# Kernel optimization log

Measured on AMD Instinct MI355X. Metric: run time of the kernel, lower is better.

## Reference

```python
import jax, jax.numpy as jnp
import numpy as np
from jax import lax

B, S, D, H_HEADS, K, G, E, HID = 2, 1024, 1024, 16, 31, 4, 2, 2048
HD = D // H_HEADS

def _layer_norm(x, g, b, eps=1e-5):
    mu = jnp.mean(x, axis=-1, keepdims=True)
    var = jnp.mean(jnp.square(x - mu), axis=-1, keepdims=True)
    return (x - mu) * lax.rsqrt(var + eps) * g + b

def setup_inputs() -> dict:
    key = jax.random.key(0)
    ks = jax.random.split(key, 16)
    s = 0.02
    return {
        "x": jax.random.normal(ks[0], (B, S, D), jnp.float32),
        "group_ids": jax.random.randint(ks[1], (B, S), 0, G, jnp.int32),
        "cn_g": jnp.ones((D,), jnp.float32), "cn_b": jnp.zeros((D,), jnp.float32),
        "conv_w": jax.random.normal(ks[2], (D, D, K), jnp.float32) * s,
        "conv_b": jnp.zeros((D,), jnp.float32),
        "an_g": jnp.ones((D,), jnp.float32), "an_b": jnp.zeros((D,), jnp.float32),
        "in_w": jax.random.normal(ks[3], (3 * D, D), jnp.float32) * s,
        "in_b": jnp.zeros((3 * D,), jnp.float32),
        "out_w": jax.random.normal(ks[4], (D, D), jnp.float32) * s,
        "out_b": jnp.zeros((D,), jnp.float32),
        "e_w1": jax.random.normal(ks[5], (G, E, D, HID), jnp.float32) * s,
        "e_b1": jnp.zeros((G, E, HID), jnp.float32),
        "e_w2": jax.random.normal(ks[6], (G, E, HID, D), jnp.float32) * s,
        "e_b2": jnp.zeros((G, E, D), jnp.float32),
    }

def reference(x, group_ids, cn_g, cn_b, conv_w, conv_b, an_g, an_b,
              in_w, in_b, out_w, out_b, e_w1, e_b1, e_w2, e_b2):
    # ---- conv block (dropout off: deterministic/eval) ----
    residual = x
    h = _layer_norm(x, cn_g, cn_b)
    hc = jnp.transpose(h, (0, 2, 1))  # [B, D, S]
    hc = lax.conv_general_dilated(hc, conv_w, window_strides=(1,),
                                  padding=[(K // 2, K // 2)],
                                  dimension_numbers=("NCH", "OIH", "NCH"))
    hc = hc + conv_b[None, :, None]
    hc = jnp.transpose(hc, (0, 2, 1))
    x = jax.nn.gelu(hc, approximate=False) + residual
    # ---- self-attention block ----
    residual = x
    h = _layer_norm(x, an_g, an_b)
    qkv = h @ in_w.T + in_b  # [B, S, 3D]
    q, k, v = jnp.split(qkv, 3, axis=-1)
    q = q.reshape(B, S, H_HEADS, HD)
    k = k.reshape(B, S, H_HEADS, HD)
    v = v.reshape(B, S, H_HEADS, HD)
    scores = jnp.einsum("bqhd,bkhd->bhqk", q, k) / jnp.sqrt(jnp.float32(HD))
    attn = jax.nn.softmax(scores, axis=-1)
    ctx = jnp.einsum("bhqk,bkhd->bqhd", attn, v).reshape(B, S, D)
    x = ctx @ out_w.T + out_b + residual
    # ---- group-routed MoE (dense compute over groups, select by group id) ----
    residual = x
    xf = x.reshape(B * S, D)
    gid = group_ids.reshape(B * S)
    h1 = jax.nn.gelu(jnp.einsum("nd,gedh->ngeh", xf, e_w1) + e_b1, approximate=False)
    out_all = jnp.einsum("ngeh,gehd->nged", h1, e_w2) + e_b2  # [N, G, E, D]
    out_all = jnp.mean(out_all, axis=2)  # mean over experts in group -> [N, G, D]
    sel = jnp.take_along_axis(out_all, gid[:, None, None].astype(jnp.int32), axis=1)[:, 0]
    x = sel.reshape(B, S, D) + residual
    return x
```

## Files before the change

kernel.cpp:

```cpp
#include <hip/hip_runtime.h>
#include <hip/hip_bf16.h>
#include <math.h>

#define BB 2
#define SS 1024
#define DD 1024
#define HH 16
#define HDIM 64
#define KK 31
#define GG 4
#define EE 2
#define HIDN 2048
#define NTOK (BB*SS)
#define D3 (3*DD)

typedef unsigned short u16;
typedef __attribute__((ext_vector_type(8))) short s16x8;
typedef __attribute__((ext_vector_type(8))) unsigned short u16x8;
typedef __attribute__((ext_vector_type(4))) unsigned short u16x4;
typedef __attribute__((ext_vector_type(4))) float f32x4;
typedef __attribute__((ext_vector_type(2))) unsigned int u32x2;

__device__ __forceinline__ float gelu_f(float x) {
  return 0.5f * x * (1.0f + erff(x * 0.7071067811865475f));
}
__device__ __forceinline__ u16 f2bf(float f) {
  unsigned u = __builtin_bit_cast(unsigned, f);
  u = (u + 0x7fffu + ((u >> 16) & 1u)) >> 16;
  return (u16)u;
}
__device__ __forceinline__ float bf2f(u16 u) {
  return __builtin_bit_cast(float, ((unsigned)u) << 16);
}
__device__ __forceinline__ f32x4 MFMA16(s16x8 a, s16x8 b, f32x4 c) {
  return __builtin_amdgcn_mfma_f32_16x16x32_bf16(a, b, c, 0, 0, 0);
}
#define GLOAD16(gp, lp) __builtin_amdgcn_global_load_lds( \
    (const __attribute__((address_space(1))) void*)(gp),  \
    (__attribute__((address_space(3))) void*)(lp), 16, 0, 0)

__global__ void ln_kernel(const float* __restrict__ x, const float* __restrict__ g,
                          const float* __restrict__ b, u16* __restrict__ out) {
  const int row = blockIdx.x;
  const int tid = threadIdx.x;
  __shared__ float red[4];
  const float4 v = reinterpret_cast<const float4*>(x + (size_t)row * DD)[tid];
  float s = v.x + v.y + v.z + v.w;
  s += __shfl_down(s, 32); s += __shfl_down(s, 16); s += __shfl_down(s, 8);
  s += __shfl_down(s, 4);  s += __shfl_down(s, 2);  s += __shfl_down(s, 1);
  if ((tid & 63) == 0) red[tid >> 6] = s;
  __syncthreads();
  const float mean = (red[0] + red[1] + red[2] + red[3]) * (1.0f / DD);
  __syncthreads();
  const float4 d = make_float4(v.x - mean, v.y - mean, v.z - mean, v.w - mean);
  float sq = d.x*d.x + d.y*d.y + d.z*d.z + d.w*d.w;
  sq += __shfl_down(sq, 32); sq += __shfl_down(sq, 16); sq += __shfl_down(sq, 8);
  sq += __shfl_down(sq, 4);  sq += __shfl_down(sq, 2);  sq += __shfl_down(sq, 1);
  if ((tid & 63) == 0) red[tid >> 6] = sq;
  __syncthreads();
  const float var = (red[0] + red[1] + red[2] + red[3]) * (1.0f / DD);
  const float rstd = rsqrtf(var + 1e-5f);
  const float4 gv = reinterpret_cast<const float4*>(g)[tid];
  const float4 bv = reinterpret_cast<const float4*>(b)[tid];
  u16x4 o;
  o[0] = f2bf(d.x * rstd * gv.x + bv.x);
  o[1] = f2bf(d.y * rstd * gv.y + bv.y);
  o[2] = f2bf(d.z * rstd * gv.z + bv.z);
  o[3] = f2bf(d.w * rstd * gv.w + bv.w);
  *reinterpret_cast<u16x4*>(out + (size_t)row * DD + tid * 4) = o;
}

__global__ void prep_convw(const float* __restrict__ cw, u16* __restrict__ Wb) {
  const int o = blockIdx.x;
  const int i4 = threadIdx.x * 4;
  float wv[4][KK];
#pragma unroll
  for (int j = 0; j < 4; ++j) {
    const float* src = cw + ((size_t)o * DD + i4 + j) * KK;
#pragma unroll
    for (int k = 0; k < KK; ++k) wv[j][k] = src[k];
  }
#pragma unroll
  for (int k = 0; k < KK; ++k) {
    u16x4 o4;
    o4[0] = f2bf(wv[0][k]); o4[1] = f2bf(wv[1][k]);
    o4[2] = f2bf(wv[2][k]); o4[3] = f2bf(wv[3][k]);
    *(u16x4*)&Wb[((size_t)k * DD + o) * DD + i4] = o4;
  }
}

__global__ void cvt_kernel(const float* __restrict__ in, u16* __restrict__ outp, int n4) {
  const int i = blockIdx.x * 256 + threadIdx.x;
  if (i < n4) {
    const float4 v = reinterpret_cast<const float4*>(in)[i];
    u16x4 o; o[0] = f2bf(v.x); o[1] = f2bf(v.y); o[2] = f2bf(v.z); o[3] = f2bf(v.w);
    reinterpret_cast<u16x4*>(outp)[i] = o;
  }
}

__global__ void tr_kernel(const float* __restrict__ src, u16* __restrict__ dst, int R, int C) {
  __shared__ float tile[32][33];
  const int c0 = blockIdx.x * 32, r0 = blockIdx.y * 32;
  const size_t base = (size_t)blockIdx.z * R * C;
  const int tx = threadIdx.x & 31, ty = threadIdx.x >> 5;
#pragma unroll
  for (int i = 0; i < 4; ++i)
    tile[ty + i * 8][tx] = src[base + (size_t)(r0 + ty + i * 8) * C + c0 + tx];
  __syncthreads();
#pragma unroll
  for (int i = 0; i < 4; ++i)
    dst[base + (size_t)(c0 + ty + i * 8) * R + r0 + tx] = f2bf(tile[tx][ty + i * 8]);
}

__global__ void vtr_kernel(const u16* __restrict__ qkvb, u16* __restrict__ Vt) {
  __shared__ u16 tile[32][40];
  const int k0 = blockIdx.x * 32, d0 = blockIdx.y * 32, bh = blockIdx.z;
  const int b = bh >> 4, h = bh & 15;
  const int tx = threadIdx.x & 31, ty = threadIdx.x >> 5;
#pragma unroll
  for (int i = 0; i < 4; ++i)
    tile[ty + i * 8][tx] =
        qkvb[(size_t)(b * SS + k0 + ty + i * 8) * D3 + 2 * DD + h * HDIM + d0 + tx];
  __syncthreads();
#pragma unroll
  for (int i = 0; i < 4; ++i)
    Vt[((size_t)(b * HH + h) * HDIM + d0 + ty + i * 8) * SS + k0 + tx] = tile[tx][ty + i * 8];
}

__global__ __launch_bounds__(512) void conv_kernel(const u16* __restrict__ hb,
                                                   const u16* __restrict__ Wb,
                                                   u16* __restrict__ P) {
  const int L = blockIdx.x;
  const int o_t = L & 7;
  const int rest = L >> 3;
  const int s_t = rest >> 1;
  const int z = rest & 1;
  const int b = s_t >> 3, sloc = s_t & 7;
  const int s0l = sloc * 128;
  const int o0 = o_t * 128;
  const int ibase = z * 512;
  const int tid = threadIdx.x, lane = tid & 63, w = tid >> 6;
  const int wm = (w >> 2) & 1, wn = (w >> 1) & 1, ksid = w & 1;
  const int q15 = lane & 15, g = lane >> 4;
  __shared__ __align__(16) u16 Ad[2][160 * 64];
  __shared__ __align__(16) u16 Bp[8][3][2048];
  const int rlo = (sloc == 0) ? 15 : 0;
  const int rhi = (sloc == 7) ? 143 : 158;
  if (sloc == 0)
    for (int i = tid; i < 15 * 64; i += 512) { Ad[0][i] = 0; Ad[1][i] = 0; }
  if (sloc == 7)
    for (int i = tid; i < 17 * 64; i += 512) { Ad[0][143 * 64 + i] = 0; Ad[1][143 * 64 + i] = 0; }
  auto stageA = [&](int buf, int i0) {
    for (int q = w; q < 20; q += 8) {
      const int r = q * 8 + (lane >> 3);
      const int c = (lane & 7) ^ (r & 7);
      if (r >= rlo && r < rhi)
        GLOAD16(hb + (size_t)(b * SS + s0l - 15 + r) * DD + i0 + c * 8, &Ad[buf][q * 512]);
    }
  };
  auto stageBp = [&](int slot, int k, int i0w) {
#pragma unroll
    for (int q = 0; q < 4; ++q) {
      const int j = lane >> 2;
      const int r = q * 16 + j;
      const int c16 = (lane & 3) ^ ((j >> 1) & 3);
      GLOAD16(Wb + ((size_t)k * DD + o0 + wn * 64 + r) * DD + i0w + c16 * 8,
              &Bp[w][slot][q * 512]);
    }
  };
  f32x4 acc[4][4];
#pragma unroll
  for (int i = 0; i < 4; ++i)
#pragma unroll
    for (int j = 0; j < 4; ++j) acc[i][j] = f32x4{0.f, 0.f, 0.f, 0.f};
  const int ib0 = ibase + ksid * 32;
  stageA(0, ibase);
  stageBp(0, 0, ib0);
  stageBp(1, 1, ib0);
  asm volatile("s_waitcnt vmcnt(0)" ::: "memory");
  __syncthreads();
  const int T = 8 * KK;
  const int kx = ksid * 64;
  const int bro = q15 * 64 + ((g ^ ((q15 >> 1) & 3)) << 4);
  int t = 0;
  for (int i0i = 0; i0i < 8; ++i0i) {
    const u16* Ab = Ad[i0i & 1];
    for (int k = 0; k < KK; ++k, ++t) {
      {
        const int tn = t + 2;
        if (tn < T) stageBp(tn % 3, tn % KK, ibase + (tn / KK) * 64 + ksid * 32);
      }
      s16x8 af[4];
      const int rk0 = wm * 64 + q15 + k;
#pragma unroll
      for (int mf = 0; mf < 4; ++mf) {
        const int rr = rk0 + mf * 16;
        const char* p = (const char*)Ab + rr * 128;
        af[mf] = *(const s16x8*)(p + (((g ^ (rr & 7)) * 16) ^ kx));
      }
      if (t + 2 < T)      asm volatile("s_waitcnt vmcnt(8)" ::: "memory");
      else if (t + 1 < T) asm volatile("s_waitcnt vmcnt(4)" ::: "memory");
      else                asm volatile("s_waitcnt vmcnt(0)" ::: "memory");
      if (k == 5 && i0i < 7) stageA((i0i + 1) & 1, ibase + (i0i + 1) * 64);
      const char* Bb = (const char*)&Bp[w][t % 3][0];
      s16x8 bfr[4];
#pragma unroll
      for (int nf = 0; nf < 4; ++nf)
        bfr[nf] = *(const s16x8*)(Bb + nf * 1024 + bro);
      __builtin_amdgcn_s_setprio(1);
#pragma unroll
      for (int mf = 0; mf < 4; ++mf)
#pragma unroll
        for (int nf = 0; nf < 4; ++nf)
          acc[mf][nf] = MFMA16(af[mf], bfr[nf], acc[mf][nf]);
      __builtin_amdgcn_s_setprio(0);
    }
    if (i0i < 7) {
      asm volatile("s_waitcnt vmcnt(0)" ::: "memory");
      __syncthreads();
    }
  }
  __syncthreads();
  float* scr = (float*)(&Bp[0][0][0]) + (wm * 2 + wn) * 4096;
  if (ksid == 1) {
#pragma unroll
    for (int mf = 0; mf < 4; ++mf)
#pragma unroll
      for (int nf = 0; nf < 4; ++nf) {
        const int col = nf * 16 + q15;
        *(f32x4*)&scr[col * 64 + ((mf * 16 + g * 4) ^ ((col & 7) << 3))] = acc[mf][nf];
      }
  }
  __syncthreads();
  if (ksid == 0) {
    u16* Pz = P + (size_t)z * NTOK * DD;
#pragma unroll
    for (int mf = 0; mf < 4; ++mf) {
      f32x4 sum[4];
#pragma unroll
      for (int nf = 0; nf < 4; ++nf) {
        const int col = nf * 16 + q15;
        const f32x4 o = *(const f32x4*)&scr[col * 64 + ((mf * 16 + g * 4) ^ ((col & 7) << 3))];
        sum[nf] = acc[mf][nf] + o;
      }
#pragma unroll
      for (int r = 0; r < 4; ++r) {
        const int srow = s0l + wm * 64 + mf * 16 + g * 4 + r;
        u16* orow = Pz + (size_t)(b * SS + srow) * DD + o0 + wn * 64;
#pragma unroll
        for (int nf = 0; nf < 4; ++nf)
          orow[nf * 16 + q15] = f2bf(sum[nf][r]);
      }
    }
  }
}

__global__ void combine_kernel(const u16* __restrict__ P, const float* __restrict__ cb,
                               const float* __restrict__ x, float* __restrict__ x1) {
  const int idx = blockIdx.x * 256 + threadIdx.x;
  const size_t base = (size_t)idx * 4;
  const int col = (int)(base & (DD - 1));
  const u16x4 p0 = *(const u16x4*)(P + base);
  const u16x4 p1 = *(const u16x4*)(P + (size_t)NTOK * DD + base);
  const float4 xv = *(const float4*)(x + base);
  const float4 cbv = *(const float4*)(cb + col);
  float4 o;
  o.x = gelu_f(bf2f(p0[0]) + bf2f(p1[0]) + cbv.x) + xv.x;
  o.y = gelu_f(bf2f(p0[1]) + bf2f(p1[1]) + cbv.y) + xv.y;
  o.z = gelu_f(bf2f(p0[2]) + bf2f(p1[2]) + cbv.z) + xv.z;
  o.w = gelu_f(bf2f(p0[3]) + bf2f(p1[3]) + cbv.w) + xv.w;
  *(float4*)(x1 + base) = o;
}

__global__ __launch_bounds__(256) void qkv_kernel(const u16* __restrict__ A, const u16* __restrict__ B,
                           const float* __restrict__ bias, u16* __restrict__ C) {
  const int n0 = blockIdx.x * 128, m0 = blockIdx.y * 128;
  const int tid = threadIdx.x, lane = tid & 63, w = tid >> 6;
  const int wm = w >> 1, wn = w & 1;
  __shared__ u16 As[2][128 * 64];
  __shared__ u16 Bs[2][128 * 64];
  f32x4 acc[4][4];
#pragma unroll
  for (int i = 0; i < 4; ++i)
#pragma unroll
    for (int j = 0; j < 4; ++j) acc[i][j] = f32x4{0.f, 0.f, 0.f, 0.f};
  auto stage = [&](int t, int buf) {
    const int k0 = t * 64;
#pragma unroll
    for (int q = 0; q < 4; ++q) {
      const int idx = w * 4 + q, r = idx * 8 + (lane >> 3), c = (lane & 7) ^ (r & 7);
      GLOAD16(A + (size_t)(m0 + r) * DD + k0 + c * 8, &As[buf][idx * 512]);
    }
#pragma unroll
    for (int q = 0; q < 4; ++q) {
      const int idx = w * 4 + q, r = idx * 8 + (lane >> 3), c = (lane & 7) ^ (r & 7);
      GLOAD16(B + (size_t)(n0 + r) * DD + k0 + c * 8, &Bs[buf][idx * 512]);
    }
  };
  stage(0, 0);
  asm volatile("s_waitcnt vmcnt(0)" ::: "memory");
  __syncthreads();
  const int T = DD / 64;
  for (int t = 0; t < T; ++t) {
    if (t > 0) {
      asm volatile("s_waitcnt vmcnt(0)" ::: "memory");
      __builtin_amdgcn_s_barrier();
      asm volatile("" ::: "memory");
    }
    if (t + 1 < T) stage(t + 1, (t + 1) & 1);
    const u16* Ab = As[t & 1];
    const u16* Bb = Bs[t & 1];
    const int xb = (((lane >> 4) ^ (lane & 7)) * 16);
    s16x8 af[4][2], bfr[4][2];
#pragma unroll
    for (int mf = 0; mf < 4; ++mf) {
      const char* p = (const char*)Ab + (wm * 64 + mf * 16 + (lane & 15)) * 128;
      af[mf][0] = *(const s16x8*)(p + xb);
      af[mf][1] = *(const s16x8*)(p + (xb ^ 64));
    }
#pragma unroll
    for (int nf = 0; nf < 4; ++nf) {
      const char* p = (const char*)Bb + (wn * 64 + nf * 16 + (lane & 15)) * 128;
      bfr[nf][0] = *(const s16x8*)(p + xb);
      bfr[nf][1] = *(const s16x8*)(p + (xb ^ 64));
    }
    __builtin_amdgcn_s_setprio(1);
#pragma unroll
    for (int ks = 0; ks < 2; ++ks)
#pragma unroll
      for (int mf = 0; mf < 4; ++mf)
#pragma unroll
        for (int nf = 0; nf < 4; ++nf)
          acc[mf][nf] = MFMA16(af[mf][ks], bfr[nf][ks], acc[mf][nf]);
    __builtin_amdgcn_s_setprio(0);
  }
#pragma unroll
  for (int mf = 0; mf < 4; ++mf)
#pragma unroll
    for (int rr = 0; rr < 4; ++rr) {
      const int row = m0 + wm * 64 + mf * 16 + (lane >> 4) * 4 + rr;
#pragma unroll
      for (int nf = 0; nf < 4; ++nf) {
        const int col = n0 + wn * 64 + nf * 16 + (lane & 15);
        C[(size_t)row * D3 + col] = f2bf(acc[mf][nf][rr] + bias[col]);
      }
    }
}

__global__ __launch_bounds__(256) void out_kernel(const u16* __restrict__ A, const u16* __restrict__ B,
                           const float* __restrict__ bias, const float* __restrict__ resid,
                           float* __restrict__ C, u16* __restrict__ x2g,
                           const int* __restrict__ inv) {
  const int n0 = blockIdx.x * 64, m0 = blockIdx.y * 128;
  const int tid = threadIdx.x, lane = tid & 63, w = tid >> 6;
  const int wm = w >> 1, wn = w & 1;
  __shared__ u16 As[3][128 * 64];
  __shared__ u16 Bs[3][64 * 64];
  f32x4 acc[4][2];
#pragma unroll
  for (int i = 0; i < 4; ++i)
#pragma unroll
    for (int j = 0; j < 2; ++j) acc[i][j] = f32x4{0.f, 0.f, 0.f, 0.f};
  auto stage = [&](int t, int buf) {
    const int k0 = t * 64;
#pragma unroll
    for (int q = 0; q < 4; ++q) {
      const int idx = w * 4 + q, r = idx * 8 + (lane >> 3), c = (lane & 7) ^ (r & 7);
      GLOAD16(A + (size_t)(m0 + r) * DD + k0 + c * 8, &As[buf][idx * 512]);
    }
#pragma unroll
    for (int q = 0; q < 2; ++q) {
      const int idx = w * 2 + q, r = idx * 8 + (lane >> 3), c = (lane & 7) ^ (r & 7);
      GLOAD16(B + (size_t)(n0 + r) * DD + k0 + c * 8, &Bs[buf][idx * 512]);
    }
  };
  stage(0, 0);
  stage(1, 1);
  const int T = DD / 64;
  for (int t = 0; t < T; ++t) {
    if (t + 1 < T) asm volatile("s_waitcnt vmcnt(6)" ::: "memory");
    else           asm volatile("s_waitcnt vmcnt(0)" ::: "memory");
    __builtin_amdgcn_s_barrier();
    asm volatile("" ::: "memory");
    if (t + 2 < T) stage(t + 2, (t + 2) % 3);
    const u16* Ab = As[t % 3];
    const u16* Bb = Bs[t % 3];
    const int xb = (((lane >> 4) ^ (lane & 7)) * 16);
    s16x8 af[4][2], bfr[2][2];
#pragma unroll
    for (int mf = 0; mf < 4; ++mf) {
      const char* p = (const char*)Ab + (wm * 64 + mf * 16 + (lane & 15)) * 128;
      af[mf][0] = *(const s16x8*)(p + xb);
      af[mf][1] = *(const s16x8*)(p + (xb ^ 64));
    }
#pragma unroll
    for (int nf = 0; nf < 2; ++nf) {
      const char* p = (const char*)Bb + (wn * 32 + nf * 16 + (lane & 15)) * 128;
      bfr[nf][0] = *(const s16x8*)(p + xb);
      bfr[nf][1] = *(const s16x8*)(p + (xb ^ 64));
    }
    __builtin_amdgcn_s_setprio(1);
#pragma unroll
    for (int ks = 0; ks < 2; ++ks)
#pragma unroll
      for (int mf = 0; mf < 4; ++mf)
#pragma unroll
        for (int nf = 0; nf < 2; ++nf)
          acc[mf][nf] = MFMA16(af[mf][ks], bfr[nf][ks], acc[mf][nf]);
    __builtin_amdgcn_s_setprio(0);
  }
#pragma unroll
  for (int mf = 0; mf < 4; ++mf)
#pragma unroll
    for (int rr = 0; rr < 4; ++rr) {
      const int row = m0 + wm * 64 + mf * 16 + (lane >> 4) * 4 + rr;
      const int slot = inv[row];
#pragma unroll
      for (int nf = 0; nf < 2; ++nf) {
        const int col = n0 + wn * 32 + nf * 16 + (lane & 15);
        const float v = acc[mf][nf][rr] + bias[col] + resid[(size_t)row * DD + col];
        C[(size_t)row * DD + col] = v;
        x2g[(size_t)slot * DD + col] = f2bf(v);
      }
    }
}

__global__ __launch_bounds__(512) void attn_kernel(const u16* __restrict__ qkv,
                                                   const u16* __restrict__ Vt,
                                                   u16* __restrict__ ctx) {
  const int q0 = blockIdx.x * 128, h = blockIdx.y, b = blockIdx.z;
  const int tid = threadIdx.x, lane = tid & 63, w = tid >> 6;
  const int q15 = lane & 15, g = lane >> 4, l7 = lane & 7;
  __shared__ u16 Q_lds[128 * 64];
  __shared__ u16 K_lds[2][64 * 64];
  __shared__ u16 V_lds[2][64 * 64];
  __shared__ u16 P_lds[8][16 * 72];
  __shared__ float s_lds[8][16];

#pragma unroll
  for (int q2 = 0; q2 < 2; ++q2) {
    const int idx = w * 2 + q2;
    const int r = idx * 8 + (lane >> 3);
    const int c = l7 ^ (r & 7);
    GLOAD16(qkv + (size_t)(b * SS + q0 + r) * D3 + h * HDIM + c * 8, &Q_lds[idx * 512]);
  }
  auto stageK = [&](int buf, int kt) {
    const int r = w * 8 + (lane >> 3);
    const int c = l7 ^ (r & 7);
    GLOAD16(qkv + (size_t)(b * SS + kt * 64 + r) * D3 + DD + h * HDIM + c * 8,
            &K_lds[buf][w * 512]);
  };
  auto stageV = [&](int buf, int kt) {
    const int r = w * 8 + (lane >> 3);
    const int c = l7 ^ (r & 7);
    GLOAD16(Vt + ((size_t)(b * HH + h) * HDIM + r) * SS + kt * 64 + c * 8,
            &V_lds[buf][w * 512]);
  };
  stageK(0, 0);
  stageV(0, 0);
  asm volatile("s_waitcnt vmcnt(0)" ::: "memory");
  __syncthreads();
  s16x8 bq[2];
#pragma unroll
  for (int ks = 0; ks < 2; ++ks)
    bq[ks] = *(const s16x8*)((const char*)Q_lds + (w * 16 + q15) * 128 + ((4 * ks + g) ^ l7) * 16);
  f32x4 oacc[4];
#pragma unroll
  for (int nf = 0; nf < 4; ++nf) oacc[nf] = f32x4{0.f, 0.f, 0.f, 0.f};
  float mrun = -3.0e38f, lrun = 0.0f;
  int buf = 0;
  for (int kt = 0; kt < 16; ++kt) {
    if (kt < 15) { stageK(buf ^ 1, kt + 1); stageV(buf ^ 1, kt + 1); }
    f32x4 st[4];
#pragma unroll
    for (int mf = 0; mf < 4; ++mf) st[mf] = f32x4{0.f, 0.f, 0.f, 0.f};
#pragma unroll
    for (int ks = 0; ks < 2; ++ks) {
#pragma unroll
      for (int mf = 0; mf < 4; ++mf) {
        const s16x8 ka = *(const s16x8*)((const char*)K_lds[buf] + (mf * 16 + q15) * 128 +
                                         ((4 * ks + g) ^ l7) * 16);
        st[mf] = MFMA16(ka, bq[ks], st[mf]);
      }
    }
    float t0[4][4];
    float cmax = -3.0e38f;
#pragma unroll
    for (int mf = 0; mf < 4; ++mf)
#pragma unroll
      for (int r = 0; r < 4; ++r) {
        const float v = st[mf][r] * 0.125f;
        t0[mf][r] = v;
        cmax = fmaxf(cmax, v);
      }
    cmax = fmaxf(cmax, __shfl_xor(cmax, 16));
    cmax = fmaxf(cmax, __shfl_xor(cmax, 32));
    const float mnew = fmaxf(mrun, cmax);
    const float scf = __expf(mrun - mnew);
    float psum = 0.f;
#pragma unroll
    for (int mf = 0; mf < 4; ++mf)
#pragma unroll
      for (int r = 0; r < 4; ++r) {
        const float p = __expf(t0[mf][r] - mnew);
        t0[mf][r] = p;
        psum += p;
      }
    psum += __shfl_xor(psum, 16);
    psum += __shfl_xor(psum, 32);
    lrun = lrun * scf + psum;
    mrun = mnew;
    s_lds[w][q15] = scf;
    u16* pw = &P_lds[w][0];
#pragma unroll
    for (int mf = 0; mf < 4; ++mf) {
      u32x2 pk;
      pk[0] = (unsigned)f2bf(t0[mf][0]) | ((unsigned)f2bf(t0[mf][1]) << 16);
      pk[1] = (unsigned)f2bf(t0[mf][2]) | ((unsigned)f2bf(t0[mf][3]) << 16);
      *(u32x2*)(pw + q15 * 72 + mf * 16 + g * 4) = pk;
    }
    asm volatile("s_waitcnt lgkmcnt(0)" ::: "memory");
    const f32x4 scv = *(const f32x4*)&s_lds[w][g * 4];
#pragma unroll
    for (int nf = 0; nf < 4; ++nf)
#pragma unroll
      for (int r = 0; r < 4; ++r) oacc[nf][r] *= scv[r];
#pragma unroll
    for (int ks = 0; ks < 2; ++ks) {
      const s16x8 pa = *(const s16x8*)(pw + q15 * 72 + ks * 32 + g * 8);
#pragma unroll
      for (int nf = 0; nf < 4; ++nf) {
        const s16x8 bv = *(const s16x8*)((const char*)V_lds[buf] + (nf * 16 + q15) * 128 +
                                         ((4 * ks + g) ^ l7) * 16);
        oacc[nf] = MFMA16(pa, bv, oacc[nf]);
      }
    }
    asm volatile("s_waitcnt vmcnt(0)" ::: "memory");
    __syncthreads();
    buf ^= 1;
  }
  const float linv = 1.0f / lrun;
  s_lds[w][q15] = linv;
  asm volatile("s_waitcnt lgkmcnt(0)" ::: "memory");
  const f32x4 lv = *(const f32x4*)&s_lds[w][g * 4];
#pragma unroll
  for (int nf = 0; nf < 4; ++nf)
#pragma unroll
    for (int r = 0; r < 4; ++r) {
      const int qg = q0 + w * 16 + g * 4 + r;
      ctx[(size_t)(b * SS + qg) * DD + h * HDIM + nf * 16 + q15] = f2bf(oacc[nf][r] * lv[r]);
    }
}

__global__ void zero_counts_kernel(int* c) { if (threadIdx.x < GG) c[threadIdx.x] = 0; }

__global__ void gather_kernel(const int* __restrict__ gid, int* __restrict__ counts,
                              int* __restrict__ gather) {
  const int n = blockIdx.x * 256 + threadIdx.x;
  if (n < NTOK) {
    const int g = gid[n];
    const int slot = atomicAdd(&counts[g], 1);
    gather[g * NTOK + slot] = n;
  }
}

__global__ void scan_kernel(const int* __restrict__ cnts, int* __restrict__ off) {
  if (threadIdx.x == 0) {
    int s = 0;
#pragma unroll
    for (int g = 0; g < GG; ++g) { off[g] = s; s += cnts[g]; }
    off[GG] = s;
  }
}

__global__ void pack_kernel(const int* __restrict__ gat, const int* __restrict__ cnts,
                            const int* __restrict__ off, int* __restrict__ gidx,
                            int* __restrict__ inv) {
  const int g = blockIdx.y;
  const int slot = blockIdx.x * 256 + threadIdx.x;
  if (slot < cnts[g]) {
    const int tok = gat[g * NTOK + slot];
    const int sg = off[g] + slot;
    gidx[sg] = tok;
    inv[tok] = sg;
  }
}

__global__ __launch_bounds__(256) void moe1_kernel(const u16* __restrict__ x2g, const u16* __restrict__ w1t,
                            const float* __restrict__ e_b1, const int* __restrict__ off,
                            const int* __restrict__ cnts, u16* __restrict__ h1) {
  const int ge = blockIdx.z, g = ge >> 1, e = ge & 1;
  const int cnt = cnts[g];
  const int m0 = blockIdx.y * 128;
  if (m0 >= cnt) return;
  const int base = off[g];
  const int n0 = blockIdx.x * 128;
  const u16* A = x2g + (size_t)base * DD;
  const u16* B = w1t + (size_t)ge * HIDN * DD;
  const int tid = threadIdx.x, lane = tid & 63, w = tid >> 6;
  const int wm = w >> 1, wn = w & 1;
  __shared__ u16 As[2][128 * 64];
  __shared__ u16 Bs[2][128 * 64];
  f32x4 acc[4][4];
#pragma unroll
  for (int i = 0; i < 4; ++i)
#pragma unroll
    for (int j = 0; j < 4; ++j) acc[i][j] = f32x4{0.f, 0.f, 0.f, 0.f};
  auto stage = [&](int t, int buf) {
    const int k0 = t * 64;
#pragma unroll
    for (int q = 0; q < 4; ++q) {
      const int idx = w * 4 + q, r = idx * 8 + (lane >> 3), c = (lane & 7) ^ (r & 7);
      int rg = m0 + r; if (rg > cnt - 1) rg = cnt - 1;
      GLOAD16(A + (size_t)rg * DD + k0 + c * 8, &As[buf][idx * 512]);
    }
#pragma unroll
    for (int q = 0; q < 4; ++q) {
      const int idx = w * 4 + q, r = idx * 8 + (lane >> 3), c = (lane & 7) ^ (r & 7);
      GLOAD16(B + (size_t)(n0 + r) * DD + k0 + c * 8, &Bs[buf][idx * 512]);
    }
  };
  stage(0, 0);
  asm volatile("s_waitcnt vmcnt(0)" ::: "memory");
  __syncthreads();
  const int T = DD / 64;
  for (int t = 0; t < T; ++t) {
    if (t > 0) {
      asm volatile("s_waitcnt vmcnt(0)" ::: "memory");
      __builtin_amdgcn_s_barrier();
      asm volatile("" ::: "memory");
    }
    if (t + 1 < T) stage(t + 1, (t + 1) & 1);
    const u16* Ab = As[t & 1];
    const u16* Bb = Bs[t & 1];
    const int xb = (((lane >> 4) ^ (lane & 7)) * 16);
    s16x8 af[4][2], bfr[4][2];
#pragma unroll
    for (int mf = 0; mf < 4; ++mf) {
      const char* p = (const char*)Ab + (wm * 64 + mf * 16 + (lane & 15)) * 128;
      af[mf][0] = *(const s16x8*)(p + xb);
      af[mf][1] = *(const s16x8*)(p + (xb ^ 64));
    }
#pragma unroll
    for (int nf = 0; nf < 4; ++nf) {
      const char* p = (const char*)Bb + (wn * 64 + nf * 16 + (lane & 15)) * 128;
      bfr[nf][0] = *(const s16x8*)(p + xb);
      bfr[nf][1] = *(const s16x8*)(p + (xb ^ 64));
    }
    __builtin_amdgcn_s_setprio(1);
#pragma unroll
    for (int ks = 0; ks < 2; ++ks)
#pragma unroll
      for (int mf = 0; mf < 4; ++mf)
#pragma unroll
        for (int nf = 0; nf < 4; ++nf)
          acc[mf][nf] = MFMA16(af[mf][ks], bfr[nf][ks], acc[mf][nf]);
    __builtin_amdgcn_s_setprio(0);
  }
  const float* b1 = e_b1 + (size_t)ge * HIDN;
#pragma unroll
  for (int mf = 0; mf < 4; ++mf)
#pragma unroll
    for (int rr = 0; rr < 4; ++rr) {
      const int rowg = m0 + wm * 64 + mf * 16 + (lane >> 4) * 4 + rr;
      if (rowg < cnt) {
        u16* orow = h1 + ((size_t)e * NTOK + base + rowg) * HIDN;
#pragma unroll
        for (int nf = 0; nf < 4; ++nf) {
          const int col = n0 + wn * 64 + nf * 16 + (lane & 15);
          orow[col] = f2bf(gelu_f(acc[mf][nf][rr] + b1[col]));
        }
      }
    }
}

__global__ __launch_bounds__(256) void moe2_kernel(const u16* __restrict__ h1, const u16* __restrict__ w2t,
                            const float* __restrict__ e_b2, const int* __restrict__ off,
                            const int* __restrict__ cnts, const int* __restrict__ gidx,
                            const float* __restrict__ x2, float* __restrict__ outp) {
  const int g = blockIdx.z;
  const int cnt = cnts[g];
  const int m0 = blockIdx.y * 128;
  if (m0 >= cnt) return;
  const int base = off[g];
  const int n0 = blockIdx.x * 64;
  const int tid = threadIdx.x, lane = tid & 63, w = tid >> 6;
  const int wm = w >> 1, wn = w & 1;
  __shared__ u16 As[3][128 * 64];
  __shared__ u16 Bs[3][64 * 64];
  f32x4 acc[4][2];
#pragma unroll
  for (int i = 0; i < 4; ++i)
#pragma unroll
    for (int j = 0; j < 2; ++j) acc[i][j] = f32x4{0.f, 0.f, 0.f, 0.f};
  auto stage = [&](int t, int buf) {
    const int e = t >> 5;
    const int k0 = (t & 31) * 64;
#pragma unroll
    for (int q = 0; q < 4; ++q) {
      const int idx = w * 4 + q, r = idx * 8 + (lane >> 3), c = (lane & 7) ^ (r & 7);
      int rg = m0 + r; if (rg > cnt - 1) rg = cnt - 1;
      GLOAD16(h1 + ((size_t)e * NTOK + base + rg) * HIDN + k0 + c * 8, &As[buf][idx * 512]);
    }
#pragma unroll
    for (int q = 0; q < 2; ++q) {
      const int idx = w * 2 + q, r = idx * 8 + (lane >> 3), c = (lane & 7) ^ (r & 7);
      GLOAD16(w2t + ((size_t)(g * EE + e) * DD + n0 + r) * HIDN + k0 + c * 8, &Bs[buf][idx * 512]);
    }
  };
  stage(0, 0);
  stage(1, 1);
  const int T = 64;
  for (int t = 0; t < T; ++t) {
    if (t + 1 < T) asm volatile("s_waitcnt vmcnt(6)" ::: "memory");
    else           asm volatile("s_waitcnt vmcnt(0)" ::: "memory");
    __builtin_amdgcn_s_barrier();
    asm volatile("" ::: "memory");
    if (t + 2 < T) stage(t + 2, (t + 2) % 3);
    const u16* Ab = As[t % 3];
    const u16* Bb = Bs[t % 3];
    const int xb = (((lane >> 4) ^ (lane & 7)) * 16);
    s16x8 af[4][2], bfr[2][2];
#pragma unroll
    for (int mf = 0; mf < 4; ++mf) {
      const char* p = (const char*)Ab + (wm * 64 + mf * 16 + (lane & 15)) * 128;
      af[mf][0] = *(const s16x8*)(p + xb);
      af[mf][1] = *(const s16x8*)(p + (xb ^ 64));
    }
#pragma unroll
    for (int nf = 0; nf < 2; ++nf) {
      const char* p = (const char*)Bb + (wn * 32 + nf * 16 + (lane & 15)) * 128;
      bfr[nf][0] = *(const s16x8*)(p + xb);
      bfr[nf][1] = *(const s16x8*)(p + (xb ^ 64));
    }
    __builtin_amdgcn_s_setprio(1);
#pragma unroll
    for (int ks = 0; ks < 2; ++ks)
#pragma unroll
      for (int mf = 0; mf < 4; ++mf)
#pragma unroll
        for (int nf = 0; nf < 2; ++nf)
          acc[mf][nf] = MFMA16(af[mf][ks], bfr[nf][ks], acc[mf][nf]);
    __builtin_amdgcn_s_setprio(0);
  }
  const float* b20 = e_b2 + (size_t)(g * EE + 0) * DD;
  const float* b21 = e_b2 + (size_t)(g * EE + 1) * DD;
#pragma unroll
  for (int mf = 0; mf < 4; ++mf)
#pragma unroll
    for (int rr = 0; rr < 4; ++rr) {
      const int rowg = m0 + wm * 64 + mf * 16 + (lane >> 4) * 4 + rr;
      if (rowg < cnt) {
        const int tok = gidx[base + rowg];
#pragma unroll
        for (int nf = 0; nf < 2; ++nf) {
          const int col = n0 + wn * 32 + nf * 16 + (lane & 15);
          outp[(size_t)tok * DD + col] =
              0.5f * acc[mf][nf][rr] + 0.5f * (b20[col] + b21[col]) + x2[(size_t)tok * DD + col];
        }
      }
    }
}

extern "C" void kernel_launch(void* const* d_in, const int* in_sizes, int n_in,
                              void* d_out, int out_size, void* d_ws, size_t ws_size,
                              hipStream_t stream) {
  (void)in_sizes; (void)n_in; (void)out_size; (void)ws_size;
  const float* x      = (const float*)d_in[0];
  const int*   gid    = (const int*)d_in[1];
  const float* cn_g   = (const float*)d_in[2];
  const float* cn_b   = (const float*)d_in[3];
  const float* conv_w = (const float*)d_in[4];
  const float* conv_b = (const float*)d_in[5];
  const float* an_g   = (const float*)d_in[6];
  const float* an_b   = (const float*)d_in[7];
  const float* in_w   = (const float*)d_in[8];
  const float* in_b   = (const float*)d_in[9];
  const float* out_w  = (const float*)d_in[10];
  const float* out_b  = (const float*)d_in[11];
  const float* e_w1   = (const float*)d_in[12];
  const float* e_b1   = (const float*)d_in[13];
  const float* e_w2   = (const float*)d_in[14];
  const float* e_b2   = (const float*)d_in[15];
  float* outp = (float*)d_out;

  char* wsp = (char*)d_ws;
  u16*   hb    = (u16*)(wsp);
  u16*   Pc    = (u16*)(wsp + (4ull << 20));
  float* x1    = (float*)(wsp + (12ull << 20));
  u16*   Wb    = (u16*)(wsp + (12ull << 20));
  u16*   qkvb  = (u16*)(wsp + (24ull << 20));
  u16*   inwb  = (u16*)(wsp + (40ull << 20));
  u16*   outwb = (u16*)(wsp + (40ull << 20));
  u16*   Vt    = (u16*)(wsp + (46ull << 20));
  u16*   ctxb  = hb;
  float* x2    = (float*)(wsp + (52ull << 20));
  int*   inv   = (int*)(wsp + (60ull << 20));
  u16*   x2g   = (u16*)(wsp + (64ull << 20));
  u16*   wgt   = (u16*)(wsp + (4ull << 20));
  u16*   h1    = (u16*)(wsp + (36ull << 20));
  int*   gat   = (int*)(wsp + (74ull << 20));
  int*   cnts  = gat + GG * NTOK;
  int*   offp  = cnts + GG;
  int*   gidx  = offp + (GG + 1);

  ln_kernel<<<NTOK, 256, 0, stream>>>(x, cn_g, cn_b, hb);
  prep_convw<<<1024, 256, 0, stream>>>(conv_w, Wb);
  conv_kernel<<<256, 512, 0, stream>>>(hb, Wb, Pc);
  combine_kernel<<<NTOK * DD / 1024, 256, 0, stream>>>(Pc, conv_b, x, x1);
  zero_counts_kernel<<<1, 64, 0, stream>>>(cnts);
  gather_kernel<<<NTOK / 256, 256, 0, stream>>>(gid, cnts, gat);
  scan_kernel<<<1, 64, 0, stream>>>(cnts, offp);
  pack_kernel<<<dim3(NTOK / 256, GG), 256, 0, stream>>>(gat, cnts, offp, gidx, inv);
  ln_kernel<<<NTOK, 256, 0, stream>>>(x1, an_g, an_b, hb);
  cvt_kernel<<<3072, 256, 0, stream>>>(in_w, inwb, 3 * DD * DD / 4);
  qkv_kernel<<<dim3(D3 / 128, NTOK / 128), 256, 0, stream>>>(hb, inwb, in_b, qkvb);
  vtr_kernel<<<dim3(SS / 32, HDIM / 32, BB * HH), 256, 0, stream>>>(qkvb, Vt);
  attn_kernel<<<dim3(SS / 128, HH, BB), 512, 0, stream>>>(qkvb, Vt, ctxb);
  cvt_kernel<<<1024, 256, 0, stream>>>(out_w, outwb, DD * DD / 4);
  out_kernel<<<dim3(DD / 64, NTOK / 128), 256, 0, stream>>>(ctxb, outwb, out_b, x1, x2, x2g, inv);
  tr_kernel<<<dim3(HIDN / 32, DD / 32, GG * EE), 256, 0, stream>>>(e_w1, wgt, DD, HIDN);
  moe1_kernel<<<dim3(HIDN / 128, NTOK / 128, GG * EE), 256, 0, stream>>>(x2g, wgt, e_b1, offp, cnts, h1);
  tr_kernel<<<dim3(DD / 32, HIDN / 32, GG * EE), 256, 0, stream>>>(e_w2, wgt, HIDN, DD);
  moe2_kernel<<<dim3(DD / 64, NTOK / 128, GG), 256, 0, stream>>>(h1, wgt, e_b2, offp, cnts, gidx, x2, outp);
}
```

Measured before the change: 489.4 us.

## Fuse attention LayerNorm into combine, merge routing kernels, widen transpose stores

The conv combine kernel now runs one block per row and also computes the attention-block LayerNorm, writing the bf16 normalized activations directly. This removes a separate LN pass that re-read x1. The four routing kernels (zero, gather, scan, pack) are replaced by a single 1024-thread block using shared-memory atomics, which cuts launch overhead. The weight transpose kernel now writes pairs of bf16 values per store. The single-block routing kernel is serial but tiny.

```diff
diff --git a/kernel.cpp b/kernel.cpp
--- a/kernel.cpp
+++ b/kernel.cpp
@@ -18,6 +18,7 @@
 typedef __attribute__((ext_vector_type(8))) short s16x8;
 typedef __attribute__((ext_vector_type(8))) unsigned short u16x8;
 typedef __attribute__((ext_vector_type(4))) unsigned short u16x4;
+typedef __attribute__((ext_vector_type(2))) unsigned short u16x2;
 typedef __attribute__((ext_vector_type(4))) float f32x4;
 typedef __attribute__((ext_vector_type(2))) unsigned int u32x2;
 
@@ -107,9 +108,15 @@
   for (int i = 0; i < 4; ++i)
     tile[ty + i * 8][tx] = src[base + (size_t)(r0 + ty + i * 8) * C + c0 + tx];
   __syncthreads();
-#pragma unroll
-  for (int i = 0; i < 4; ++i)
-    dst[base + (size_t)(c0 + ty + i * 8) * R + r0 + tx] = f2bf(tile[tx][ty + i * 8]);
+  const int rx = threadIdx.x & 15, cy = threadIdx.x >> 4;
+#pragma unroll
+  for (int i = 0; i < 2; ++i) {
+    const int c = cy + i * 16;
+    u16x2 o2;
+    o2[0] = f2bf(tile[2 * rx][c]);
+    o2[1] = f2bf(tile[2 * rx + 1][c]);
+    *(u16x2*)&dst[base + (size_t)(c0 + c) * R + r0 + 2 * rx] = o2;
+  }
 }
 
 __global__ void vtr_kernel(const u16* __restrict__ qkvb, u16* __restrict__ Vt) {
@@ -256,20 +263,47 @@
 }
 
 __global__ void combine_kernel(const u16* __restrict__ P, const float* __restrict__ cb,
-                               const float* __restrict__ x, float* __restrict__ x1) {
-  const int idx = blockIdx.x * 256 + threadIdx.x;
-  const size_t base = (size_t)idx * 4;
-  const int col = (int)(base & (DD - 1));
+                               const float* __restrict__ x, const float* __restrict__ an_g,
+                               const float* __restrict__ an_b, float* __restrict__ x1,
+                               u16* __restrict__ hb) {
+  const int row = blockIdx.x;
+  const int tid = threadIdx.x;
+  const size_t base = (size_t)row * DD + tid * 4;
+  const int col = tid * 4;
+  __shared__ float red[4];
   const u16x4 p0 = *(const u16x4*)(P + base);
   const u16x4 p1 = *(const u16x4*)(P + (size_t)NTOK * DD + base);
   const float4 xv = *(const float4*)(x + base);
   const float4 cbv = *(const float4*)(cb + col);
-  float4 o;
-  o.x = gelu_f(bf2f(p0[0]) + bf2f(p1[0]) + cbv.x) + xv.x;
-  o.y = gelu_f(bf2f(p0[1]) + bf2f(p1[1]) + cbv.y) + xv.y;
-  o.z = gelu_f(bf2f(p0[2]) + bf2f(p1[2]) + cbv.z) + xv.z;
-  o.w = gelu_f(bf2f(p0[3]) + bf2f(p1[3]) + cbv.w) + xv.w;
-  *(float4*)(x1 + base) = o;
+  float4 v;
+  v.x = gelu_f(bf2f(p0[0]) + bf2f(p1[0]) + cbv.x) + xv.x;
+  v.y = gelu_f(bf2f(p0[1]) + bf2f(p1[1]) + cbv.y) + xv.y;
+  v.z = gelu_f(bf2f(p0[2]) + bf2f(p1[2]) + cbv.z) + xv.z;
+  v.w = gelu_f(bf2f(p0[3]) + bf2f(p1[3]) + cbv.w) + xv.w;
+  *(float4*)(x1 + base) = v;
+  float s = v.x + v.y + v.z + v.w;
+  s += __shfl_down(s, 32); s += __shfl_down(s, 16); s += __shfl_down(s, 8);
+  s += __shfl_down(s, 4);  s += __shfl_down(s, 2);  s += __shfl_down(s, 1);
+  if ((tid & 63) == 0) red[tid >> 6] = s;
+  __syncthreads();
+  const float mean = (red[0] + red[1] + red[2] + red[3]) * (1.0f / DD);
+  __syncthreads();
+  const float4 d = make_float4(v.x - mean, v.y - mean, v.z - mean, v.w - mean);
+  float sq = d.x*d.x + d.y*d.y + d.z*d.z + d.w*d.w;
+  sq += __shfl_down(sq, 32); sq += __shfl_down(sq, 16); sq += __shfl_down(sq, 8);
+  sq += __shfl_down(sq, 4);  sq += __shfl_down(sq, 2);  sq += __shfl_down(sq, 1);
+  if ((tid & 63) == 0) red[tid >> 6] = sq;
+  __syncthreads();
+  const float var = (red[0] + red[1] + red[2] + red[3]) * (1.0f / DD);
+  const float rstd = rsqrtf(var + 1e-5f);
+  const float4 gv = reinterpret_cast<const float4*>(an_g)[tid];
+  const float4 bv = reinterpret_cast<const float4*>(an_b)[tid];
+  u16x4 o;
+  o[0] = f2bf(d.x * rstd * gv.x + bv.x);
+  o[1] = f2bf(d.y * rstd * gv.y + bv.y);
+  o[2] = f2bf(d.z * rstd * gv.z + bv.z);
+  o[3] = f2bf(d.w * rstd * gv.w + bv.w);
+  *reinterpret_cast<u16x4*>(hb + (size_t)row * DD + tid * 4) = o;
 }
 
 __global__ __launch_bounds__(256) void qkv_kernel(const u16* __restrict__ A, const u16* __restrict__ B,
@@ -552,38 +586,32 @@
     }
 }
 
-__global__ void zero_counts_kernel(int* c) { if (threadIdx.x < GG) c[threadIdx.x] = 0; }
-
-__global__ void gather_kernel(const int* __restrict__ gid, int* __restrict__ counts,
-                              int* __restrict__ gather) {
-  const int n = blockIdx.x * 256 + threadIdx.x;
-  if (n < NTOK) {
-    const int g = gid[n];
-    const int slot = atomicAdd(&counts[g], 1);
-    gather[g * NTOK + slot] = n;
-  }
-}
-
-__global__ void scan_kernel(const int* __restrict__ cnts, int* __restrict__ off) {
-  if (threadIdx.x == 0) {
+__global__ void routing_kernel(const int* __restrict__ gid, int* __restrict__ cnts_g,
+                               int* __restrict__ off_g, int* __restrict__ gidx,
+                               int* __restrict__ inv) {
+  __shared__ int cnt[GG];
+  __shared__ int off[GG + 1];
+  const int tid = threadIdx.x;
+  if (tid < GG) cnt[tid] = 0;
+  __syncthreads();
+  const int t0 = tid, t1 = tid + 1024;
+  const int g0 = gid[t0], g1 = gid[t1];
+  const int s0 = atomicAdd(&cnt[g0], 1);
+  const int s1 = atomicAdd(&cnt[g1], 1);
+  __syncthreads();
+  if (tid == 0) {
     int s = 0;
 #pragma unroll
-    for (int g = 0; g < GG; ++g) { off[g] = s; s += cnts[g]; }
+    for (int g = 0; g < GG; ++g) { off[g] = s; s += cnt[g]; }
     off[GG] = s;
   }
-}
-
-__global__ void pack_kernel(const int* __restrict__ gat, const int* __restrict__ cnts,
-                            const int* __restrict__ off, int* __restrict__ gidx,
-                            int* __restrict__ inv) {
-  const int g = blockIdx.y;
-  const int slot = blockIdx.x * 256 + threadIdx.x;
-  if (slot < cnts[g]) {
-    const int tok = gat[g * NTOK + slot];
-    const int sg = off[g] + slot;
-    gidx[sg] = tok;
-    inv[tok] = sg;
-  }
+  __syncthreads();
+  const int sg0 = off[g0] + s0;
+  gidx[sg0] = t0; inv[t0] = sg0;
+  const int sg1 = off[g1] + s1;
+  gidx[sg1] = t1; inv[t1] = sg1;
+  if (tid < GG) cnts_g[tid] = cnt[tid];
+  if (tid <= GG) off_g[tid] = off[tid];
 }
 
 __global__ __launch_bounds__(256) void moe1_kernel(const u16* __restrict__ x2g, const u16* __restrict__ w1t,
@@ -807,12 +835,8 @@
   ln_kernel<<<NTOK, 256, 0, stream>>>(x, cn_g, cn_b, hb);
   prep_convw<<<1024, 256, 0, stream>>>(conv_w, Wb);
   conv_kernel<<<256, 512, 0, stream>>>(hb, Wb, Pc);
-  combine_kernel<<<NTOK * DD / 1024, 256, 0, stream>>>(Pc, conv_b, x, x1);
-  zero_counts_kernel<<<1, 64, 0, stream>>>(cnts);
-  gather_kernel<<<NTOK / 256, 256, 0, stream>>>(gid, cnts, gat);
-  scan_kernel<<<1, 64, 0, stream>>>(cnts, offp);
-  pack_kernel<<<dim3(NTOK / 256, GG), 256, 0, stream>>>(gat, cnts, offp, gidx, inv);
-  ln_kernel<<<NTOK, 256, 0, stream>>>(x1, an_g, an_b, hb);
+  combine_kernel<<<NTOK, 256, 0, stream>>>(Pc, conv_b, x, an_g, an_b, x1, hb);
+  routing_kernel<<<1, 1024, 0, stream>>>(gid, cnts, offp, gidx, inv);
   cvt_kernel<<<3072, 256, 0, stream>>>(in_w, inwb, 3 * DD * DD / 4);
   qkv_kernel<<<dim3(D3 / 128, NTOK / 128), 256, 0, stream>>>(hb, inwb, in_b, qkvb);
   vtr_kernel<<<dim3(SS / 32, HDIM / 32, BB * HH), 256, 0, stream>>>(qkvb, Vt);
```

Result: faster. 472.0 us (-3.6%).
